# Optimization experiments

Measured on AMD Instinct MI355X. Metric: run time of the kernel, lower is better.

## Reference

```python
import jax, jax.numpy as jnp
import numpy as np

N_NODES = 100000
N_EDGES = 1600000
NEG_SLOPE = 0.2
EPS = 1e-16


def _gat_layer(x, src, dst, W, att_src, att_dst, bias, heads, out_ch):
    # x: [N, F_in]; src/dst: [E'] (self-loops already appended)
    n = x.shape[0]
    h = (x @ W).reshape(n, heads, out_ch)                      # [N, H, C]
    a_src = (h * att_src[None]).sum(-1)                        # [N, H]
    a_dst = (h * att_dst[None]).sum(-1)                        # [N, H]
    e = a_src[src] + a_dst[dst]                                # [E', H]
    e = jnp.where(e > 0, e, NEG_SLOPE * e)                     # leaky_relu
    # segment softmax over incoming edges of each dst node
    m = jax.ops.segment_max(e, dst, num_segments=n)            # [N, H]
    ex = jnp.exp(e - m[dst])                                   # [E', H]
    s = jax.ops.segment_sum(ex, dst, num_segments=n)           # [N, H]
    alpha = ex / (s[dst] + EPS)                                # [E', H]
    msg = h[src] * alpha[:, :, None]                           # [E', H, C]
    out = jax.ops.segment_sum(msg, dst, num_segments=n)        # [N, H, C]
    return out.reshape(n, heads * out_ch) + bias


def setup_inputs() -> dict:
    key = jax.random.key(0)
    ks = jax.random.split(key, 10)
    x = jax.random.normal(ks[0], (N_NODES, 165), dtype=jnp.float32)
    src = jax.random.randint(ks[1], (N_EDGES,), 0, N_NODES, dtype=jnp.int32)
    dst = jax.random.randint(ks[2], (N_EDGES,), 0, N_NODES, dtype=jnp.int32)
    glorot = lambda k, shp: jax.random.normal(k, shp, dtype=jnp.float32) * jnp.sqrt(2.0 / (shp[0] + shp[-1]))
    W1 = glorot(ks[3], (165, 256))
    att_src1 = glorot(ks[4], (4, 64))
    att_dst1 = glorot(ks[5], (4, 64))
    b1 = jnp.zeros((256,), dtype=jnp.float32)
    W2 = glorot(ks[6], (256, 2))
    att_src2 = glorot(ks[7], (1, 2))
    att_dst2 = glorot(ks[8], (1, 2))
    b2 = jnp.zeros((2,), dtype=jnp.float32)
    return {"x": x, "src": src, "dst": dst,
            "W1": W1, "att_src1": att_src1, "att_dst1": att_dst1, "b1": b1,
            "W2": W2, "att_src2": att_src2, "att_dst2": att_dst2, "b2": b2}


def reference(x, src, dst, W1, att_src1, att_dst1, b1, W2, att_src2, att_dst2, b2):
    n = x.shape[0]
    # PyG GATConv adds self-loops by default
    loops = jnp.arange(n, dtype=src.dtype)
    s = jnp.concatenate([src, loops])
    d = jnp.concatenate([dst, loops])
    h = _gat_layer(x, s, d, W1, att_src1, att_dst1, b1, heads=4, out_ch=64)
    h = jax.nn.relu(h)
    # F.dropout with training=False is identity (eval mode)
    out = _gat_layer(h, s, d, W2, att_src2, att_dst2, b2, heads=1, out_ch=2)
    return jax.nn.log_softmax(out, axis=1)
```

## Files before the change

kernel.cpp:

```cpp
#include <hip/hip_runtime.h>
#include <math.h>

#define NN 100000
#define NE 1600000
#define ET (NE + NN)
#define NEG 0.2f
#define KP 192
#define GEMM_BLKS (NN / 32)
#define SLOTS 64
#define NPART 8
#define PART_SZ (NN / NPART)
#define NCHUNK 1024
#define CH ((NE + NCHUNK - 1) / NCHUNK)
#define HS_BLKS (NPART * NCHUNK)
#define LDA 200

typedef __attribute__((ext_vector_type(8))) short short8;
typedef __attribute__((ext_vector_type(4))) float floatx4;

__device__ __forceinline__ unsigned short f2bf(float f) {
    unsigned u = __float_as_uint(f);
    unsigned r = u + 0x7fffu + ((u >> 16) & 1u);
    return (unsigned short)(r >> 16);
}
__device__ __forceinline__ float bflo(unsigned x) { return __uint_as_float(x << 16); }
__device__ __forceinline__ float bfhi(unsigned x) { return __uint_as_float(x & 0xFFFF0000u); }

__global__ __launch_bounds__(256) void k_prep(const float* __restrict__ W,
                                              unsigned short* __restrict__ Wt,
                                              int* __restrict__ deg,
                                              int* __restrict__ esrc) {
    const int gid = blockIdx.x * 256 + threadIdx.x;
    const int G = gridDim.x * 256;
    for (int idx = gid; idx < 256 * KP; idx += G) {
        const int n = idx / KP, k = idx - n * KP;
        Wt[idx] = (k < 165) ? f2bf(W[k * 256 + n]) : (unsigned short)0;
    }
    for (int i = gid; i < NN; i += G) { deg[i] = 1; esrc[i << 6] = i; }
}

__global__ __launch_bounds__(256, 5) void k_hsgemm(const int* __restrict__ src,
                                                const int* __restrict__ dst,
                                                const float* __restrict__ x,
                                                const unsigned short* __restrict__ Wt,
                                                const float* __restrict__ att_s,
                                                const float* __restrict__ att_d,
                                                int* __restrict__ deg,
                                                int* __restrict__ esrc,
                                                unsigned short* __restrict__ h1,
                                                float* __restrict__ a_src,
                                                float* __restrict__ a_dst) {
    __shared__ __align__(16) unsigned lds_u32[32 * 132];
    const int t = threadIdx.x;
    const int b = blockIdx.x;

    if (b < HS_BLKS) {
        const int p = b & 7;
        const int chunk = b >> 3;
        const int e0 = chunk * CH;
        const int e1 = (e0 + CH < NE) ? e0 + CH : NE;
        const int plo = p * PART_SZ, phi = plo + PART_SZ;
        for (int e = e0 + t; e < e1; e += 256) {
            const int d = dst[e];
            if (d >= plo && d < phi) {
                const int s = src[e];
                const int r = atomicAdd(&deg[d], 1);
                if (r < SLOTS) esrc[(d << 6) + r] = s;
            }
        }
        return;
    }

    const int n0 = (b - HS_BLKS) * 32;
    unsigned short* lds_a = (unsigned short*)lds_u32;

    for (int i = t; i < 32 * 165; i += 256) {
        const int n = i / 165, k = i - n * 165;
        lds_a[n * LDA + k] = f2bf(x[(size_t)(n0 + n) * 165 + k]);
    }
    for (int i = t; i < 32 * (LDA - 165); i += 256) {
        const int n = i / (LDA - 165), k = 165 + (i - n * (LDA - 165));
        lds_a[n * LDA + k] = 0;
    }
    __syncthreads();

    const int lane = t & 63, hd = t >> 6;
    const int r16 = lane & 15, quad = lane >> 4;
    floatx4 zero4 = {0.0f, 0.0f, 0.0f, 0.0f};
    floatx4 acc[2][4];
#pragma unroll
    for (int mm = 0; mm < 2; ++mm)
#pragma unroll
        for (int nn = 0; nn < 4; ++nn) acc[mm][nn] = zero4;

    const unsigned short* ar0 = lds_a + r16 * LDA;
    const unsigned short* ar1 = lds_a + (16 + r16) * LDA;
#pragma unroll
    for (int ks = 0; ks < 6; ++ks) {
        const int kb = ks * 32 + quad * 8;
        short8 a0 = *(const short8*)(ar0 + kb);
        short8 a1 = *(const short8*)(ar1 + kb);
#pragma unroll
        for (int nn = 0; nn < 4; ++nn) {
            short8 bf = *(const short8*)(Wt + (size_t)(hd * 64 + nn * 16 + r16) * KP + kb);
            acc[0][nn] = __builtin_amdgcn_mfma_f32_16x16x32_bf16(a0, bf, acc[0][nn], 0, 0, 0);
            acc[1][nn] = __builtin_amdgcn_mfma_f32_16x16x32_bf16(a1, bf, acc[1][nn], 0, 0, 0);
        }
    }

    float asw[4], adw[4];
#pragma unroll
    for (int nn = 0; nn < 4; ++nn) {
        asw[nn] = att_s[hd * 64 + nn * 16 + r16];
        adw[nn] = att_d[hd * 64 + nn * 16 + r16];
    }
#pragma unroll
    for (int mm = 0; mm < 2; ++mm)
#pragma unroll
        for (int r = 0; r < 4; ++r) {
            float ps = acc[mm][0][r] * asw[0] + acc[mm][1][r] * asw[1] +
                       acc[mm][2][r] * asw[2] + acc[mm][3][r] * asw[3];
            float pd = acc[mm][0][r] * adw[0] + acc[mm][1][r] * adw[1] +
                       acc[mm][2][r] * adw[2] + acc[mm][3][r] * adw[3];
            ps += __shfl_xor(ps, 1); ps += __shfl_xor(ps, 2);
            ps += __shfl_xor(ps, 4); ps += __shfl_xor(ps, 8);
            pd += __shfl_xor(pd, 1); pd += __shfl_xor(pd, 2);
            pd += __shfl_xor(pd, 4); pd += __shfl_xor(pd, 8);
            if (r16 == 0) {
                const int node = n0 + mm * 16 + quad * 4 + r;
                a_src[node * 4 + hd] = ps;
                a_dst[node * 4 + hd] = pd;
            }
        }

    __syncthreads();
#pragma unroll
    for (int mm = 0; mm < 2; ++mm)
#pragma unroll
        for (int nn = 0; nn < 4; ++nn)
#pragma unroll
            for (int r = 0; r < 4; ++r) {
                const float v = acc[mm][nn][r];
                const float o = __shfl_xor(v, 1);
                if ((lane & 1) == 0) {
                    const unsigned pk = (unsigned)f2bf(v) | ((unsigned)f2bf(o) << 16);
                    lds_u32[(mm * 16 + quad * 4 + r) * 132 + hd * 32 + nn * 8 + (r16 >> 1)] = pk;
                }
            }
    __syncthreads();
    {
        const int row = t & 31, seg = t >> 5;
        const unsigned* p = &lds_u32[row * 132 + seg * 16];
        uint4 d0 = *(const uint4*)(p);
        uint4 d1 = *(const uint4*)(p + 4);
        uint4 d2 = *(const uint4*)(p + 8);
        uint4 d3 = *(const uint4*)(p + 12);
        unsigned short* hp = h1 + (size_t)(n0 + row) * 256 + seg * 32;
        *(uint4*)(hp) = d0;
        *(uint4*)(hp + 8) = d1;
        *(uint4*)(hp + 16) = d2;
        *(uint4*)(hp + 24) = d3;
    }
}

__global__ __launch_bounds__(256) void k_l1agg(const unsigned short* __restrict__ h1,
                                               const float* __restrict__ a_src,
                                               const float* __restrict__ a_dst,
                                               const int* __restrict__ deg,
                                               const int* __restrict__ esrc,
                                               const float* __restrict__ b1,
                                               const float* __restrict__ W2,
                                               const float* __restrict__ att_s2,
                                               const float* __restrict__ att_d2,
                                               float4* __restrict__ node2) {
    const int t = threadIdx.x;
    const int n = blockIdx.x * 4 + (t >> 6);
    const int l = t & 63;
    const int q = l >> 4;
    const int sl = l & 15;
    const int head = sl >> 2;
    const int c0 = sl * 16;
    const int el = l >> 2;
    const int hl = l & 3;
    const int dg = deg[n];
    const int ebase = n << 6;
    const float4 ad4 = *(const float4*)&a_dst[n * 4];
    const float adh = (hl == 0) ? ad4.x : (hl == 1) ? ad4.y : (hl == 2) ? ad4.z : ad4.w;

    float ssum = 0.0f;
    float acc[16];
#pragma unroll
    for (int c = 0; c < 16; ++c) acc[c] = 0.0f;

    for (int base = 0; base < dg; base += 16) {
        const int cnt = dg - base;
        const int iters = (cnt < 16) ? cnt : 16;
        int sA = 0; float pA = 0.0f;
        if (el < cnt) {
            sA = esrc[ebase + base + el];
            const float a = a_src[sA * 4 + hl] + adh;
            const float e = (a > 0.0f) ? a : NEG * a;
            pA = __expf(e);
        }
#pragma unroll
        for (int jb = 0; jb < 16; jb += 4) {
            const int j = jb + q;
            const int s = __shfl(sA, j << 2);
            const float p = __shfl(pA, (j << 2) | head);
            if (j < iters) {
                ssum += p;
                const unsigned ho = ((unsigned)s << 8) + c0;
                const uint4 hv0 = *(const uint4*)(h1 + ho);
                const uint4 hv1 = *(const uint4*)(h1 + ho + 8);
                acc[0]  += p * bflo(hv0.x); acc[1]  += p * bfhi(hv0.x);
                acc[2]  += p * bflo(hv0.y); acc[3]  += p * bfhi(hv0.y);
                acc[4]  += p * bflo(hv0.z); acc[5]  += p * bfhi(hv0.z);
                acc[6]  += p * bflo(hv0.w); acc[7]  += p * bfhi(hv0.w);
                acc[8]  += p * bflo(hv1.x); acc[9]  += p * bfhi(hv1.x);
                acc[10] += p * bflo(hv1.y); acc[11] += p * bfhi(hv1.y);
                acc[12] += p * bflo(hv1.z); acc[13] += p * bfhi(hv1.z);
                acc[14] += p * bflo(hv1.w); acc[15] += p * bfhi(hv1.w);
            }
        }
    }
    ssum += __shfl_xor(ssum, 16); ssum += __shfl_xor(ssum, 32);
#pragma unroll
    for (int c = 0; c < 16; ++c) {
        acc[c] += __shfl_xor(acc[c], 16);
        acc[c] += __shfl_xor(acc[c], 32);
    }
    const float inv = 1.0f / ssum;
    float p0 = 0.0f, p1 = 0.0f;
#pragma unroll
    for (int c = 0; c < 16; ++c) {
        const float v = fmaxf(acc[c] * inv + b1[c0 + c], 0.0f);
        p0 += v * W2[(c0 + c) * 2 + 0];
        p1 += v * W2[(c0 + c) * 2 + 1];
    }
    if (q) { p0 = 0.0f; p1 = 0.0f; }
#pragma unroll
    for (int off = 32; off; off >>= 1) {
        p0 += __shfl_down(p0, off);
        p1 += __shfl_down(p1, off);
    }
    if (l == 0) {
        const float as2v = p0 * att_s2[0] + p1 * att_s2[1];
        const float ad2v = p0 * att_d2[0] + p1 * att_d2[1];
        node2[n] = make_float4(p0, p1, as2v, ad2v);
    }
}

__global__ __launch_bounds__(256) void k_l2agg(const float4* __restrict__ node2,
                                               const int* __restrict__ deg,
                                               const int* __restrict__ esrc,
                                               const float* __restrict__ b2,
                                               float* __restrict__ out) {
    const int t = threadIdx.x;
    const int l = t & 63;
    const int g = l >> 4;
    const int i = l & 15;
    const int n = blockIdx.x * 16 + (t >> 6) * 4 + g;
    const int dg = deg[n];
    const int ebase = n << 6;
    const float adst = node2[n].w;
    float ssum = 0.0f, a0 = 0.0f, a1 = 0.0f;
    for (int idx = i; idx < dg; idx += 16) {
        const int s = esrc[ebase + idx];
        const float4 r = node2[s];
        const float a = r.z + adst;
        const float e = (a > 0.0f) ? a : NEG * a;
        const float p = __expf(e);
        ssum += p; a0 += p * r.x; a1 += p * r.y;
    }
#pragma unroll
    for (int off = 8; off; off >>= 1) {
        ssum += __shfl_xor(ssum, off);
        a0 += __shfl_xor(a0, off);
        a1 += __shfl_xor(a1, off);
    }
    if (i == 0) {
        const float inv = 1.0f / ssum;
        const float z0 = a0 * inv + b2[0];
        const float z1 = a1 * inv + b2[1];
        const float mz = fmaxf(z0, z1);
        const float lse = mz + __logf(__expf(z0 - mz) + __expf(z1 - mz));
        out[n * 2 + 0] = z0 - lse;
        out[n * 2 + 1] = z1 - lse;
    }
}

extern "C" void kernel_launch(void* const* d_in, const int* in_sizes, int n_in,
                              void* d_out, int out_size, void* d_ws, size_t ws_size,
                              hipStream_t stream) {
    const float* x    = (const float*)d_in[0];
    const int*   src  = (const int*)d_in[1];
    const int*   dst  = (const int*)d_in[2];
    const float* W1   = (const float*)d_in[3];
    const float* as1w = (const float*)d_in[4];
    const float* ad1w = (const float*)d_in[5];
    const float* b1   = (const float*)d_in[6];
    const float* W2   = (const float*)d_in[7];
    const float* as2w = (const float*)d_in[8];
    const float* ad2w = (const float*)d_in[9];
    const float* b2   = (const float*)d_in[10];
    float* out = (float*)d_out;

    char* w = (char*)d_ws;
    unsigned short* h1  = (unsigned short*)w; w += (size_t)NN * 256 * 2;
    unsigned short* Wt  = (unsigned short*)w; w += (size_t)256 * KP * 2;
    float* a_src = (float*)w; w += (size_t)NN * 4 * 4;
    float* a_dst = (float*)w; w += (size_t)NN * 4 * 4;
    float4* node2 = (float4*)w; w += (size_t)NN * 4 * 4;
    int* deg     = (int*)w;   w += (size_t)NN * 4;
    int* esrc    = (int*)w;   w += (size_t)NN * SLOTS * 4;

    k_prep<<<512, 256, 0, stream>>>(W1, Wt, deg, esrc);
    k_hsgemm<<<HS_BLKS + GEMM_BLKS, 256, 0, stream>>>(src, dst, x, Wt, as1w, ad1w,
                                                      deg, esrc, h1, a_src, a_dst);
    k_l1agg<<<NN / 4, 256, 0, stream>>>(h1, a_src, a_dst, deg, esrc, b1, W2, as2w, ad2w, node2);
    k_l2agg<<<NN / 16, 256, 0, stream>>>(node2, deg, esrc, b2, out);
}
```

Baseline: 412.3 us.

## Split GEMM into per-row-tile passes, drop LDS staging, remap hist blocks

The fused GEMM kernel now handles its two 16-row tiles one after another, so only four accumulators are live at a time. Occupancy goes from 5 to 6 blocks per CU, the LDS output staging buffer is dropped, and each lane writes packed bf16 pairs straight to global memory. The edge-bucketing blocks are remapped so consecutive blocks share a partition and walk adjacent chunks, which changes atomic locality. The cost is that Wt fragments are reloaded for each row tile, and the global stores are narrow 4-byte ones instead of 16-byte coalesced rows.

```diff
diff --git a/kernel.cpp b/kernel.cpp
--- a/kernel.cpp
+++ b/kernel.cpp
@@ -39,7 +39,7 @@
     for (int i = gid; i < NN; i += G) { deg[i] = 1; esrc[i << 6] = i; }
 }
 
-__global__ __launch_bounds__(256, 5) void k_hsgemm(const int* __restrict__ src,
+__global__ __launch_bounds__(256, 6) void k_hsgemm(const int* __restrict__ src,
                                                 const int* __restrict__ dst,
                                                 const float* __restrict__ x,
                                                 const unsigned short* __restrict__ Wt,
@@ -50,13 +50,13 @@
                                                 unsigned short* __restrict__ h1,
                                                 float* __restrict__ a_src,
                                                 float* __restrict__ a_dst) {
-    __shared__ __align__(16) unsigned lds_u32[32 * 132];
+    __shared__ __align__(16) unsigned short lds_a[32 * LDA];
     const int t = threadIdx.x;
     const int b = blockIdx.x;
 
     if (b < HS_BLKS) {
-        const int p = b & 7;
-        const int chunk = b >> 3;
+        const int p = b >> 10;
+        const int chunk = b & 1023;
         const int e0 = chunk * CH;
         const int e1 = (e0 + CH < NE) ? e0 + CH : NE;
         const int plo = p * PART_SZ, phi = plo + PART_SZ;
@@ -72,7 +72,6 @@
     }
 
     const int n0 = (b - HS_BLKS) * 32;
-    unsigned short* lds_a = (unsigned short*)lds_u32;
 
     for (int i = t; i < 32 * 165; i += 256) {
         const int n = i / 165, k = i - n * 165;
@@ -86,42 +85,38 @@
 
     const int lane = t & 63, hd = t >> 6;
     const int r16 = lane & 15, quad = lane >> 4;
-    floatx4 zero4 = {0.0f, 0.0f, 0.0f, 0.0f};
-    floatx4 acc[2][4];
-#pragma unroll
-    for (int mm = 0; mm < 2; ++mm)
-#pragma unroll
-        for (int nn = 0; nn < 4; ++nn) acc[mm][nn] = zero4;
-
-    const unsigned short* ar0 = lds_a + r16 * LDA;
-    const unsigned short* ar1 = lds_a + (16 + r16) * LDA;
-#pragma unroll
-    for (int ks = 0; ks < 6; ++ks) {
-        const int kb = ks * 32 + quad * 8;
-        short8 a0 = *(const short8*)(ar0 + kb);
-        short8 a1 = *(const short8*)(ar1 + kb);
-#pragma unroll
-        for (int nn = 0; nn < 4; ++nn) {
-            short8 bf = *(const short8*)(Wt + (size_t)(hd * 64 + nn * 16 + r16) * KP + kb);
-            acc[0][nn] = __builtin_amdgcn_mfma_f32_16x16x32_bf16(a0, bf, acc[0][nn], 0, 0, 0);
-            acc[1][nn] = __builtin_amdgcn_mfma_f32_16x16x32_bf16(a1, bf, acc[1][nn], 0, 0, 0);
-        }
-    }
-
     float asw[4], adw[4];
 #pragma unroll
     for (int nn = 0; nn < 4; ++nn) {
         asw[nn] = att_s[hd * 64 + nn * 16 + r16];
         adw[nn] = att_d[hd * 64 + nn * 16 + r16];
     }
-#pragma unroll
-    for (int mm = 0; mm < 2; ++mm)
+
+#pragma unroll
+    for (int mm = 0; mm < 2; ++mm) {
+        floatx4 acc[4];
+        floatx4 zero4 = {0.0f, 0.0f, 0.0f, 0.0f};
+#pragma unroll
+        for (int nn = 0; nn < 4; ++nn) acc[nn] = zero4;
+
+        const unsigned short* ar = lds_a + (mm * 16 + r16) * LDA;
+#pragma unroll
+        for (int ks = 0; ks < 6; ++ks) {
+            const int kb = ks * 32 + quad * 8;
+            short8 a = *(const short8*)(ar + kb);
+#pragma unroll
+            for (int nn = 0; nn < 4; ++nn) {
+                short8 bf = *(const short8*)(Wt + (size_t)(hd * 64 + nn * 16 + r16) * KP + kb);
+                acc[nn] = __builtin_amdgcn_mfma_f32_16x16x32_bf16(a, bf, acc[nn], 0, 0, 0);
+            }
+        }
+
 #pragma unroll
         for (int r = 0; r < 4; ++r) {
-            float ps = acc[mm][0][r] * asw[0] + acc[mm][1][r] * asw[1] +
-                       acc[mm][2][r] * asw[2] + acc[mm][3][r] * asw[3];
-            float pd = acc[mm][0][r] * adw[0] + acc[mm][1][r] * adw[1] +
-                       acc[mm][2][r] * adw[2] + acc[mm][3][r] * adw[3];
+            float ps = acc[0][r] * asw[0] + acc[1][r] * asw[1] +
+                       acc[2][r] * asw[2] + acc[3][r] * asw[3];
+            float pd = acc[0][r] * adw[0] + acc[1][r] * adw[1] +
+                       acc[2][r] * adw[2] + acc[3][r] * adw[3];
             ps += __shfl_xor(ps, 1); ps += __shfl_xor(ps, 2);
             ps += __shfl_xor(ps, 4); ps += __shfl_xor(ps, 8);
             pd += __shfl_xor(pd, 1); pd += __shfl_xor(pd, 2);
@@ -133,33 +128,18 @@
             }
         }
 
-    __syncthreads();
-#pragma unroll
-    for (int mm = 0; mm < 2; ++mm)
 #pragma unroll
         for (int nn = 0; nn < 4; ++nn)
 #pragma unroll
             for (int r = 0; r < 4; ++r) {
-                const float v = acc[mm][nn][r];
+                const float v = acc[nn][r];
                 const float o = __shfl_xor(v, 1);
                 if ((lane & 1) == 0) {
                     const unsigned pk = (unsigned)f2bf(v) | ((unsigned)f2bf(o) << 16);
-                    lds_u32[(mm * 16 + quad * 4 + r) * 132 + hd * 32 + nn * 8 + (r16 >> 1)] = pk;
+                    const int node = n0 + mm * 16 + quad * 4 + r;
+                    *(unsigned*)(h1 + (size_t)node * 256 + hd * 64 + nn * 16 + r16) = pk;
                 }
             }
-    __syncthreads();
-    {
-        const int row = t & 31, seg = t >> 5;
-        const unsigned* p = &lds_u32[row * 132 + seg * 16];
-        uint4 d0 = *(const uint4*)(p);
-        uint4 d1 = *(const uint4*)(p + 4);
-        uint4 d2 = *(const uint4*)(p + 8);
-        uint4 d3 = *(const uint4*)(p + 12);
-        unsigned short* hp = h1 + (size_t)(n0 + row) * 256 + seg * 32;
-        *(uint4*)(hp) = d0;
-        *(uint4*)(hp + 8) = d1;
-        *(uint4*)(hp + 16) = d2;
-        *(uint4*)(hp + 24) = d3;
     }
 }
 
```

New measurement: 460.8 us. 11.8% more time.
